# Kernel tuning notes

Measured on AMD Instinct MI355X. Metric: run time of the kernel, lower is better.

## Reference

```python
import jax, jax.numpy as jnp
import numpy as np
import math

B, L, D, H = 8, 1000, 1024, 16
HD = D // H

def setup_inputs() -> dict:
    key = jax.random.key(0)
    k1, k2, k3 = jax.random.split(key, 3)
    s_in = 1.0 / math.sqrt(D)
    x = jax.random.normal(k1, (B, L, D), dtype=jnp.float32)
    Wqkv = jax.random.normal(k2, (D, 3 * D), dtype=jnp.float32) * s_in
    bqkv = jnp.zeros((3 * D,), dtype=jnp.float32)
    Wo = jax.random.normal(k3, (D, D), dtype=jnp.float32) * s_in
    bo = jnp.zeros((D,), dtype=jnp.float32)
    return {"x": x, "Wqkv": Wqkv, "bqkv": bqkv, "Wo": Wo, "bo": bo}

def reference(x, Wqkv, bqkv, Wo, bo):
    b, l, d = x.shape
    qkv = x @ Wqkv + bqkv                      # [B,L,3D]
    q, k, v = jnp.split(qkv, 3, axis=-1)       # each [B,L,D]
    q = q.reshape(b, l, H, HD)
    k = k.reshape(b, l, H, HD)
    v = v.reshape(b, l, H, HD)
    scale = 1.0 / math.sqrt(HD)
    att = jnp.einsum('blhd,bmhd->bhlm', q, k) * scale   # [B,H,L,L]
    causal = jnp.tril(jnp.ones((l, l), dtype=bool))      # [L,L]
    att = jnp.where(causal[None, None, :, :], att, -jnp.inf)
    att = jax.nn.softmax(att, axis=-1)
    out = jnp.einsum('bhlm,bmhd->blhd', att, v).reshape(b, l, d)
    return out @ Wo + bo
```

## Files before the change

kernel.cpp:

```cpp
#include <hip/hip_runtime.h>
#include <hip/hip_bf16.h>

typedef unsigned short u16;
typedef unsigned int u32;
typedef __attribute__((ext_vector_type(8))) __bf16 bf16x8;
typedef __attribute__((ext_vector_type(4))) float f32x4;
typedef __attribute__((ext_vector_type(4))) u16 u16x4;

#define LQ 1000
#define MM 8000

__device__ __forceinline__ u16 f2bf(float f){
  __bf16 h = (__bf16)f;
  return __builtin_bit_cast(u16, h);
}
__device__ __forceinline__ void async_copy16(const void* g, void* l){
  __builtin_amdgcn_global_load_lds((const __attribute__((address_space(1))) u32*)g,
                                   (__attribute__((address_space(3))) u32*)l, 16, 0, 0);
}

__device__ __forceinline__ void ttile(const float* __restrict__ src, u16* __restrict__ dst,
                                      int R, int C, int bxt, int byt, u16 (*tile)[33]){
  const int tx = threadIdx.x & 31, ty = threadIdx.x >> 5;
  const long bx = (long)bxt * 32, by = (long)byt * 32;
  #pragma unroll
  for (int i = 0; i < 32; i += 8) tile[ty + i][tx] = f2bf(src[(by + ty + i) * C + bx + tx]);
  __syncthreads();
  #pragma unroll
  for (int i = 0; i < 32; i += 8) dst[(bx + ty + i) * R + by + tx] = tile[tx][ty + i];
}

__global__ __launch_bounds__(256)
void kprep(const float* __restrict__ x, u16* __restrict__ xb,
           const float* __restrict__ Wqkv, u16* __restrict__ WqkvT,
           const float* __restrict__ Wo, u16* __restrict__ WoT)
{
  __shared__ u16 tile[32][33];
  const int bid = blockIdx.x;
  if (bid < 2048) {
    const int t = threadIdx.x;
    for (long base = (long)bid * 1024; base < 8192000L; base += 2048L * 1024) {
      const long i = base + t * 4;
      const float4 v = *(const float4*)&x[i];
      u16x4 o; o.x = f2bf(v.x); o.y = f2bf(v.y); o.z = f2bf(v.z); o.w = f2bf(v.w);
      *(u16x4*)&xb[i] = o;
    }
  } else if (bid < 5120) {
    const int idx = bid - 2048;
    ttile(Wqkv, WqkvT, 1024, 3072, idx % 96, idx / 96, tile);
  } else {
    const int idx = bid - 5120;
    ttile(Wo, WoT, 1024, 1024, idx % 32, idx / 32, tile);
  }
}

template<int EPI, int BN>
__global__ __launch_bounds__(256)
void gemm128(const u16* __restrict__ A, const u16* __restrict__ BT, const float* __restrict__ bias,
             u16* __restrict__ O0, u16* __restrict__ O1, u16* __restrict__ O2,
             float* __restrict__ OF)
{
  constexpr int K = 1024;
  constexpr int NF = BN / 32;
  __shared__ __align__(16) u16 As[2][128 * 32];
  __shared__ __align__(16) u16 Bs[2][BN * 32];
  const int t = threadIdx.x, lane = t & 63, wave = t >> 6;
  const int quad = lane >> 4, l15 = lane & 15;
  const int m0 = blockIdx.y * 128, n0 = blockIdx.x * BN;
  const int wm = (wave >> 1) * 64, wn = (wave & 1) * (BN / 2);

  f32x4 acc[4][NF] = {};

  const int srow = t >> 2;
  const int sg   = (t & 3) ^ ((srow >> 1) & 3);
  const int scol = sg * 8;
  const long aoff0 = (long)min(m0 + srow,      MM - 1) * K + scol;
  const long aoff1 = (long)min(m0 + srow + 64, MM - 1) * K + scol;
  const long boff0 = (long)(n0 + srow)      * K + scol;
  const long boff1 = (long)(n0 + srow + 64) * K + scol;
  char* AsB0 = (char*)As[0] + wave * 1024;
  char* AsB1 = (char*)As[1] + wave * 1024;
  char* BsB0 = (char*)Bs[0] + wave * 1024;
  char* BsB1 = (char*)Bs[1] + wave * 1024;

  const int swz = (l15 >> 1) & 3;

  for (int kt = 0; kt < K; kt += 64) {
    __syncthreads();
    async_copy16(A  + aoff0 + kt,      AsB0);
    async_copy16(A  + aoff1 + kt,      AsB0 + 4096);
    async_copy16(BT + boff0 + kt,      BsB0);
    if constexpr (BN == 128) async_copy16(BT + boff1 + kt,      BsB0 + 4096);
    async_copy16(A  + aoff0 + kt + 32, AsB1);
    async_copy16(A  + aoff1 + kt + 32, AsB1 + 4096);
    async_copy16(BT + boff0 + kt + 32, BsB1);
    if constexpr (BN == 128) async_copy16(BT + boff1 + kt + 32, BsB1 + 4096);
    __syncthreads();
    #pragma unroll
    for (int half = 0; half < 2; half++) {
      bf16x8 af[4], bfv[NF];
      #pragma unroll
      for (int i = 0; i < 4; i++)  af[i]  = *(const bf16x8*)&As[half][(wm + i * 16 + l15) * 32 + (quad ^ swz) * 8];
      #pragma unroll
      for (int i = 0; i < NF; i++) bfv[i] = *(const bf16x8*)&Bs[half][(wn + i * 16 + l15) * 32 + (quad ^ swz) * 8];
      #pragma unroll
      for (int mi = 0; mi < 4; mi++)
        #pragma unroll
        for (int ni = 0; ni < NF; ni++)
          acc[mi][ni] = __builtin_amdgcn_mfma_f32_16x16x32_bf16(af[mi], bfv[ni], acc[mi][ni], 0, 0, 0);
    }
  }

  float bs[NF]; int cols[NF];
  #pragma unroll
  for (int ni = 0; ni < NF; ni++) { cols[ni] = n0 + wn + ni * 16 + l15; bs[ni] = bias[cols[ni]]; }

  #pragma unroll
  for (int mi = 0; mi < 4; mi++) {
    #pragma unroll
    for (int r = 0; r < 4; r++) {
      const int row = m0 + wm + mi * 16 + quad * 4 + r;
      if (row >= MM) continue;
      if (EPI == 0) {
        const int b = row / 1000, l = row - b * 1000;
        #pragma unroll
        for (int ni = 0; ni < NF; ni++) {
          const u16 o = f2bf(acc[mi][ni][r] + bs[ni]);
          const int col = cols[ni];
          const int which = col >> 10, hh = (col >> 6) & 15, dd = col & 63;
          const int bh = b * 16 + hh;
          if      (which == 0) O0[((long)bh * LQ + l) * 64 + dd] = o;
          else if (which == 1) O1[((long)bh * LQ + l) * 64 + dd] = o;
          else                 O2[((long)bh * 64 + dd) * LQ + l] = o;
        }
      } else {
        #pragma unroll
        for (int ni = 0; ni < NF; ni++)
          OF[(long)row * 1024 + cols[ni]] = acc[mi][ni][r] + bs[ni];
      }
    }
  }
}

__global__ __launch_bounds__(128)
void gemmN(const u16* __restrict__ A, const u16* __restrict__ BT, const float* __restrict__ bias,
           float* __restrict__ OF)
{
  constexpr int K = 1024;
  __shared__ __align__(16) u16 As[2][64 * 32];
  __shared__ __align__(16) u16 Bs[2][128 * 32];
  const int t = threadIdx.x, lane = t & 63, wave = t >> 6;
  const int quad = lane >> 4, l15 = lane & 15;
  const int m0 = blockIdx.y * 64, n0 = blockIdx.x * 128;
  const int wn = wave * 64;

  f32x4 acc[4][4] = {};

  const int srl = lane >> 2;
  const int sg  = (lane & 3) ^ ((srl >> 1) & 3);
  const int scol = sg * 8;
  long aoff[2], boff[4];
  #pragma unroll
  for (int j = 0; j < 2; j++) aoff[j] = (long)(m0 + wave * 16 + srl + j * 32) * K + scol;
  #pragma unroll
  for (int j = 0; j < 4; j++) boff[j] = (long)(n0 + wave * 16 + srl + j * 32) * K + scol;

  const int swz = (l15 >> 1) & 3;

  for (int kt = 0; kt < K; kt += 64) {
    __syncthreads();
    #pragma unroll
    for (int half = 0; half < 2; half++) {
      char* Ad = (char*)As[half] + wave * 1024;
      char* Bd = (char*)Bs[half] + wave * 1024;
      const int ko = kt + half * 32;
      #pragma unroll
      for (int j = 0; j < 2; j++) async_copy16(A + aoff[j] + ko, Ad + j * 2048);
      #pragma unroll
      for (int j = 0; j < 4; j++) async_copy16(BT + boff[j] + ko, Bd + j * 2048);
    }
    __syncthreads();
    #pragma unroll
    for (int half = 0; half < 2; half++) {
      bf16x8 af[4], bfv[4];
      #pragma unroll
      for (int i = 0; i < 4; i++) af[i]  = *(const bf16x8*)&As[half][(i * 16 + l15) * 32 + (quad ^ swz) * 8];
      #pragma unroll
      for (int i = 0; i < 4; i++) bfv[i] = *(const bf16x8*)&Bs[half][(wn + i * 16 + l15) * 32 + (quad ^ swz) * 8];
      #pragma unroll
      for (int mi = 0; mi < 4; mi++)
        #pragma unroll
        for (int ni = 0; ni < 4; ni++)
          acc[mi][ni] = __builtin_amdgcn_mfma_f32_16x16x32_bf16(af[mi], bfv[ni], acc[mi][ni], 0, 0, 0);
    }
  }

  float bs[4]; int cols[4];
  #pragma unroll
  for (int ni = 0; ni < 4; ni++) { cols[ni] = n0 + wn + ni * 16 + l15; bs[ni] = bias[cols[ni]]; }

  #pragma unroll
  for (int mi = 0; mi < 4; mi++) {
    #pragma unroll
    for (int r = 0; r < 4; r++) {
      const int row = m0 + mi * 16 + quad * 4 + r;
      #pragma unroll
      for (int ni = 0; ni < 4; ni++)
        OF[(long)row * 1024 + cols[ni]] = acc[mi][ni][r] + bs[ni];
    }
  }
}

__global__ __launch_bounds__(256)
void attn_kernel(const u16* __restrict__ Qb, const u16* __restrict__ Kb,
                 const u16* __restrict__ VTb, u16* __restrict__ AO)
{
  __shared__ __align__(16) u16 Ps[4][2][16 * 40];
  const int t = threadIdx.x, lane = t & 63, wave = t >> 6;
  const int quad = lane >> 4, l15 = lane & 15;
  const int lin = blockIdx.y * 4 + blockIdx.x;
  const int swz = (lin & 7) * 64 + (lin >> 3);
  const int bh  = swz >> 2;
  const int s   = swz & 3;
  const int c   = ((wave & 2) ? 8 : 0) + ((wave & 1) ? (7 - s) : s);
  const int ch[2] = { c, 31 - c };
  const int nkt = 32 - c;
  const u16* Q  = Qb  + (long)bh * LQ * 64;
  const u16* Kp = Kb  + (long)bh * LQ * 64;
  const u16* VT = VTb + (long)bh * 64 * LQ;
  const int b = bh >> 4, h = bh & 15;
  const float sscale = 0.18033688011112042f;

  int qv[2][2]; bf16x8 bq0[2][2], bq1[2][2];
  #pragma unroll
  for (int cj = 0; cj < 2; cj++) {
    #pragma unroll
    for (int g = 0; g < 2; g++) {
      qv[cj][g] = ch[cj] * 32 + g * 16 + l15;
      const int qc = min(qv[cj][g], LQ - 1);
      bq0[cj][g] = *(const bf16x8*)&Q[(long)qc * 64 +      quad * 8];
      bq1[cj][g] = *(const bf16x8*)&Q[(long)qc * 64 + 32 + quad * 8];
    }
  }

  float l_p[2][2] = {{0.f, 0.f}, {0.f, 0.f}};
  f32x4 o[2][2][4] = {};

  bf16x8 pa00, pa01, pa10, pa11, pav0, pav1, pav2, pav3;
  {
    const int krA = min(l15, LQ - 1), krB = min(16 + l15, LQ - 1);
    pa00 = *(const bf16x8*)&Kp[(long)krA * 64 +      quad * 8];
    pa01 = *(const bf16x8*)&Kp[(long)krA * 64 + 32 + quad * 8];
    pa10 = *(const bf16x8*)&Kp[(long)krB * 64 +      quad * 8];
    pa11 = *(const bf16x8*)&Kp[(long)krB * 64 + 32 + quad * 8];
    const int vcol = min(quad * 8, LQ - 8);
    pav0 = *(const bf16x8*)&VT[(long)( 0 + l15) * LQ + vcol];
    pav1 = *(const bf16x8*)&VT[(long)(16 + l15) * LQ + vcol];
    pav2 = *(const bf16x8*)&VT[(long)(32 + l15) * LQ + vcol];
    pav3 = *(const bf16x8*)&VT[(long)(48 + l15) * LQ + vcol];
  }

  for (int kk = 0; kk < nkt; ++kk) {
    const int k0 = kk * 32;
    const bf16x8 a00 = pa00, a01 = pa01, a10 = pa10, a11 = pa11;
    bf16x8 av[4] = { pav0, pav1, pav2, pav3 };
    if (kk + 1 < nkt) {
      const int n0k = k0 + 32;
      const int krA = min(n0k + l15, LQ - 1), krB = min(n0k + 16 + l15, LQ - 1);
      pa00 = *(const bf16x8*)&Kp[(long)krA * 64 +      quad * 8];
      pa01 = *(const bf16x8*)&Kp[(long)krA * 64 + 32 + quad * 8];
      pa10 = *(const bf16x8*)&Kp[(long)krB * 64 +      quad * 8];
      pa11 = *(const bf16x8*)&Kp[(long)krB * 64 + 32 + quad * 8];
      const int vcol = min(n0k + quad * 8, LQ - 8);
      pav0 = *(const bf16x8*)&VT[(long)( 0 + l15) * LQ + vcol];
      pav1 = *(const bf16x8*)&VT[(long)(16 + l15) * LQ + vcol];
      pav2 = *(const bf16x8*)&VT[(long)(32 + l15) * LQ + vcol];
      pav3 = *(const bf16x8*)&VT[(long)(48 + l15) * LQ + vcol];
    }

    #pragma unroll
    for (int cj = 0; cj < 2; cj++) {
      if (cj == 0 && kk > ch[0]) continue;
      const bool lastt = (kk == ch[cj]);
      #pragma unroll
      for (int g = 0; g < 2; g++) {
        const f32x4 z = {};
        __builtin_amdgcn_s_setprio(1);
        f32x4 s0 = __builtin_amdgcn_mfma_f32_16x16x32_bf16(a00, bq0[cj][g], z, 0, 0, 0);
        s0       = __builtin_amdgcn_mfma_f32_16x16x32_bf16(a01, bq1[cj][g], s0, 0, 0, 0);
        f32x4 s1 = __builtin_amdgcn_mfma_f32_16x16x32_bf16(a10, bq0[cj][g], z, 0, 0, 0);
        s1       = __builtin_amdgcn_mfma_f32_16x16x32_bf16(a11, bq1[cj][g], s1, 0, 0, 0);
        __builtin_amdgcn_s_setprio(0);

        float p0[4], p1[4];
        if (lastt) {
          const int q = qv[cj][g];
          #pragma unroll
          for (int r = 0; r < 4; r++) {
            const int key0 = k0 + quad * 4 + r;
            p0[r] = __builtin_amdgcn_exp2f((key0      <= q) ? s0[r] * sscale : -3.0e38f);
            p1[r] = __builtin_amdgcn_exp2f((key0 + 16 <= q) ? s1[r] * sscale : -3.0e38f);
          }
        } else {
          #pragma unroll
          for (int r = 0; r < 4; r++) {
            p0[r] = __builtin_amdgcn_exp2f(s0[r] * sscale);
            p1[r] = __builtin_amdgcn_exp2f(s1[r] * sscale);
          }
        }
        u16x4 w0, w1; float ls = 0.f;
        #pragma unroll
        for (int r = 0; r < 4; r++) {
          w0[r] = f2bf(p0[r]); w1[r] = f2bf(p1[r]);
          ls += p0[r] + p1[r];
        }
        l_p[cj][g] += ls;
        *(u16x4*)&Ps[wave][g][l15 * 40 + quad * 4]      = w0;
        *(u16x4*)&Ps[wave][g][l15 * 40 + 16 + quad * 4] = w1;
        const bf16x8 bp = *(const bf16x8*)&Ps[wave][g][l15 * 40 + quad * 8];
        __builtin_amdgcn_s_setprio(1);
        #pragma unroll
        for (int cc = 0; cc < 4; cc++)
          o[cj][g][cc] = __builtin_amdgcn_mfma_f32_16x16x32_bf16(av[cc], bp, o[cj][g][cc], 0, 0, 0);
        __builtin_amdgcn_s_setprio(0);
      }
    }
  }

  #pragma unroll
  for (int cj = 0; cj < 2; cj++) {
    #pragma unroll
    for (int g = 0; g < 2; g++) {
      if (qv[cj][g] >= LQ) continue;
      float l = l_p[cj][g];
      l += __shfl_xor(l, 16);
      l += __shfl_xor(l, 32);
      const float inv = 1.0f / l;
      const long base = ((long)(b * LQ + qv[cj][g])) * 1024 + h * 64;
      #pragma unroll
      for (int cc = 0; cc < 4; cc++) {
        u16x4 w;
        #pragma unroll
        for (int r = 0; r < 4; r++) w[r] = f2bf(o[cj][g][cc][r] * inv);
        *(u16x4*)&AO[base + cc * 16 + quad * 4] = w;
      }
    }
  }
}

extern "C" void kernel_launch(void* const* d_in, const int* in_sizes, int n_in,
                              void* d_out, int out_size, void* d_ws, size_t ws_size,
                              hipStream_t stream) {
  const float* x    = (const float*)d_in[0];
  const float* Wqkv = (const float*)d_in[1];
  const float* bqkv = (const float*)d_in[2];
  const float* Wo   = (const float*)d_in[3];
  const float* bo   = (const float*)d_in[4];
  float* out = (float*)d_out;

  char* ws = (char*)d_ws;
  u16* WqkvT = (u16*)(ws);
  u16* WoT   = (u16*)(ws + 6291456);
  u16* xb    = (u16*)(ws + 8388608);
  u16* Qb    = (u16*)(ws + 8388608 + 16384000L);
  u16* Kb    = (u16*)(ws + 8388608 + 2 * 16384000L);
  u16* VTb   = (u16*)(ws + 8388608 + 3 * 16384000L);
  u16* AO    = xb;

  kprep<<<6144, 256, 0, stream>>>(x, xb, Wqkv, WqkvT, Wo, WoT);
  gemm128<0, 128><<<dim3(24, 63), 256, 0, stream>>>(xb, WqkvT, bqkv, Qb, Kb, VTb, nullptr);
  attn_kernel<<<dim3(4, 128), 256, 0, stream>>>(Qb, Kb, VTb, AO);
  gemmN<<<dim3(8, 125), 128, 0, stream>>>(AO, WoT, bo, out);
}
```

Before: 257.1 us.

## Use 128x128 tiles with intra-block split-K for output projection GEMM

The output projection GEMM now runs 128x128 tiles in 512-thread blocks. Two 256-thread groups each handle half of K (512), and their partial sums are reduced through shared memory before the bias add and store. The larger tile gives more operand reuse, and the split-K keeps enough waves in flight even though the grid drops to 504 blocks. The costs are 64KB of LDS per block, an extra reduction pass through LDS, and masking of rows beyond 8000 for the last tile.

```diff
diff --git a/kernel.cpp b/kernel.cpp
--- a/kernel.cpp
+++ b/kernel.cpp
@@ -142,51 +142,55 @@
   }
 }
 
-__global__ __launch_bounds__(128)
-void gemmN(const u16* __restrict__ A, const u16* __restrict__ BT, const float* __restrict__ bias,
+__global__ __launch_bounds__(512)
+void gemmO(const u16* __restrict__ A, const u16* __restrict__ BT, const float* __restrict__ bias,
            float* __restrict__ OF)
 {
-  constexpr int K = 1024;
-  __shared__ __align__(16) u16 As[2][64 * 32];
-  __shared__ __align__(16) u16 Bs[2][128 * 32];
-  const int t = threadIdx.x, lane = t & 63, wave = t >> 6;
+  __shared__ __align__(16) char smem[65536];
+  u16 (*As)[128 * 32] = (u16 (*)[128 * 32])smem;
+  u16 (*Bs)[128 * 32] = (u16 (*)[128 * 32])(smem + 32768);
+  const int grp = threadIdx.x >> 8;
+  const int t = threadIdx.x & 255;
+  const int lane = t & 63, wave = t >> 6;
   const int quad = lane >> 4, l15 = lane & 15;
-  const int m0 = blockIdx.y * 64, n0 = blockIdx.x * 128;
-  const int wn = wave * 64;
+  const int m0 = blockIdx.y * 128, n0 = blockIdx.x * 128;
+  const int wm = (wave >> 1) * 64, wn = (wave & 1) * 64;
+  const long kbase = grp * 512;
 
   f32x4 acc[4][4] = {};
 
-  const int srl = lane >> 2;
-  const int sg  = (lane & 3) ^ ((srl >> 1) & 3);
+  const int srow = t >> 2;
+  const int sg   = (t & 3) ^ ((srow >> 1) & 3);
   const int scol = sg * 8;
-  long aoff[2], boff[4];
-  #pragma unroll
-  for (int j = 0; j < 2; j++) aoff[j] = (long)(m0 + wave * 16 + srl + j * 32) * K + scol;
-  #pragma unroll
-  for (int j = 0; j < 4; j++) boff[j] = (long)(n0 + wave * 16 + srl + j * 32) * K + scol;
+  const long aoff0 = (long)min(m0 + srow,      MM - 1) * 1024 + kbase + scol;
+  const long aoff1 = (long)min(m0 + srow + 64, MM - 1) * 1024 + kbase + scol;
+  const long boff0 = (long)(n0 + srow)      * 1024 + kbase + scol;
+  const long boff1 = (long)(n0 + srow + 64) * 1024 + kbase + scol;
+  char* AsB0 = (char*)As[grp * 2 + 0] + wave * 1024;
+  char* AsB1 = (char*)As[grp * 2 + 1] + wave * 1024;
+  char* BsB0 = (char*)Bs[grp * 2 + 0] + wave * 1024;
+  char* BsB1 = (char*)Bs[grp * 2 + 1] + wave * 1024;
 
   const int swz = (l15 >> 1) & 3;
 
-  for (int kt = 0; kt < K; kt += 64) {
+  for (int kt = 0; kt < 512; kt += 64) {
     __syncthreads();
-    #pragma unroll
-    for (int half = 0; half < 2; half++) {
-      char* Ad = (char*)As[half] + wave * 1024;
-      char* Bd = (char*)Bs[half] + wave * 1024;
-      const int ko = kt + half * 32;
-      #pragma unroll
-      for (int j = 0; j < 2; j++) async_copy16(A + aoff[j] + ko, Ad + j * 2048);
-      #pragma unroll
-      for (int j = 0; j < 4; j++) async_copy16(BT + boff[j] + ko, Bd + j * 2048);
-    }
+    async_copy16(A  + aoff0 + kt,      AsB0);
+    async_copy16(A  + aoff1 + kt,      AsB0 + 4096);
+    async_copy16(BT + boff0 + kt,      BsB0);
+    async_copy16(BT + boff1 + kt,      BsB0 + 4096);
+    async_copy16(A  + aoff0 + kt + 32, AsB1);
+    async_copy16(A  + aoff1 + kt + 32, AsB1 + 4096);
+    async_copy16(BT + boff0 + kt + 32, BsB1);
+    async_copy16(BT + boff1 + kt + 32, BsB1 + 4096);
     __syncthreads();
     #pragma unroll
     for (int half = 0; half < 2; half++) {
       bf16x8 af[4], bfv[4];
       #pragma unroll
-      for (int i = 0; i < 4; i++) af[i]  = *(const bf16x8*)&As[half][(i * 16 + l15) * 32 + (quad ^ swz) * 8];
-      #pragma unroll
-      for (int i = 0; i < 4; i++) bfv[i] = *(const bf16x8*)&Bs[half][(wn + i * 16 + l15) * 32 + (quad ^ swz) * 8];
+      for (int i = 0; i < 4; i++) af[i]  = *(const bf16x8*)&As[grp * 2 + half][(wm + i * 16 + l15) * 32 + (quad ^ swz) * 8];
+      #pragma unroll
+      for (int i = 0; i < 4; i++) bfv[i] = *(const bf16x8*)&Bs[grp * 2 + half][(wn + i * 16 + l15) * 32 + (quad ^ swz) * 8];
       #pragma unroll
       for (int mi = 0; mi < 4; mi++)
         #pragma unroll
@@ -195,18 +199,38 @@
     }
   }
 
-  float bs[4]; int cols[4];
-  #pragma unroll
-  for (int ni = 0; ni < 4; ni++) { cols[ni] = n0 + wn + ni * 16 + l15; bs[ni] = bias[cols[ni]]; }
-
-  #pragma unroll
-  for (int mi = 0; mi < 4; mi++) {
-    #pragma unroll
-    for (int r = 0; r < 4; r++) {
-      const int row = m0 + mi * 16 + quad * 4 + r;
+  __syncthreads();
+  float* dump = (float*)smem;
+  if (grp == 1) {
+    #pragma unroll
+    for (int mi = 0; mi < 4; mi++)
       #pragma unroll
       for (int ni = 0; ni < 4; ni++)
-        OF[(long)row * 1024 + cols[ni]] = acc[mi][ni][r] + bs[ni];
+        *(f32x4*)&dump[(mi * 4 + ni) * 1024 + t * 4] = acc[mi][ni];
+  }
+  __syncthreads();
+  if (grp == 0) {
+    #pragma unroll
+    for (int mi = 0; mi < 4; mi++)
+      #pragma unroll
+      for (int ni = 0; ni < 4; ni++) {
+        const f32x4 p = *(const f32x4*)&dump[(mi * 4 + ni) * 1024 + t * 4];
+        acc[mi][ni] += p;
+      }
+
+    float bs[4]; int cols[4];
+    #pragma unroll
+    for (int ni = 0; ni < 4; ni++) { cols[ni] = n0 + wn + ni * 16 + l15; bs[ni] = bias[cols[ni]]; }
+    #pragma unroll
+    for (int mi = 0; mi < 4; mi++) {
+      #pragma unroll
+      for (int r = 0; r < 4; r++) {
+        const int row = m0 + wm + mi * 16 + quad * 4 + r;
+        if (row >= MM) continue;
+        #pragma unroll
+        for (int ni = 0; ni < 4; ni++)
+          OF[(long)row * 1024 + cols[ni]] = acc[mi][ni][r] + bs[ni];
+      }
     }
   }
 }
@@ -370,5 +394,5 @@
   kprep<<<6144, 256, 0, stream>>>(x, xb, Wqkv, WqkvT, Wo, WoT);
   gemm128<0, 128><<<dim3(24, 63), 256, 0, stream>>>(xb, WqkvT, bqkv, Qb, Kb, VTb, nullptr);
   attn_kernel<<<dim3(4, 128), 256, 0, stream>>>(Qb, Kb, VTb, AO);
-  gemmN<<<dim3(8, 125), 128, 0, stream>>>(AO, WoT, bo, out);
-}
+  gemmO<<<dim3(8, 63), 512, 0, stream>>>(AO, WoT, bo, out);
+}
```

After: 260.3 us. Within noise of the previous version (+1.2%).
